# Performance work log

Hardware: AMD Instinct MI355X
Metric: run time of the kernel (lower is better)

Reference implementation:

```python
import jax, jax.numpy as jnp
import numpy as np

N_NODES = 50000
N_EDGES = 800000
IN_FEAT = 128
OUT_FEAT = 128


def setup_inputs() -> dict:
    key = jax.random.key(0)
    ks = jax.random.split(key, 12)
    s = lambda fan_in: 1.0 / np.sqrt(fan_in)
    inp = {
        "node_feats": jax.random.normal(ks[0], (N_NODES, IN_FEAT), dtype=jnp.float32),
        "edge_feats": jax.random.normal(ks[1], (N_EDGES, IN_FEAT), dtype=jnp.float32),
        "src": jax.random.randint(ks[2], (N_EDGES,), 0, N_NODES),
        "dst": jax.random.randint(ks[3], (N_EDGES,), 0, N_NODES),
        # mlp1: Linear(2*in -> in), ReLU, Linear(in -> in)
        "W1a": jax.random.uniform(ks[4], (2 * IN_FEAT, IN_FEAT), jnp.float32, -s(2 * IN_FEAT), s(2 * IN_FEAT)),
        "b1a": jnp.zeros((IN_FEAT,), jnp.float32),
        "W1b": jax.random.uniform(ks[5], (IN_FEAT, IN_FEAT), jnp.float32, -s(IN_FEAT), s(IN_FEAT)),
        "b1b": jnp.zeros((IN_FEAT,), jnp.float32),
        # mlp2: Linear(in -> out), ReLU, Linear(out -> out)
        "W2a": jax.random.uniform(ks[6], (IN_FEAT, OUT_FEAT), jnp.float32, -s(IN_FEAT), s(IN_FEAT)),
        "b2a": jnp.zeros((OUT_FEAT,), jnp.float32),
        "W2b": jax.random.uniform(ks[7], (OUT_FEAT, OUT_FEAT), jnp.float32, -s(OUT_FEAT), s(OUT_FEAT)),
        "b2b": jnp.zeros((OUT_FEAT,), jnp.float32),
    }
    return inp


def reference(node_feats, edge_feats, src, dst, W1a, b1a, W1b, b1b, W2a, b2a, W2b, b2b):
    # message: mlp1(cat([h_src, e]))  -> [E, in_feat]
    cat = jnp.concatenate([node_feats[src], edge_feats], axis=1)  # [E, 2*in]
    m = jax.nn.relu(cat @ W1a + b1a) @ W1b + b1b                  # [E, in]
    # reduce: scatter-sum over dst + residual
    agg = jax.ops.segment_sum(m, dst, num_segments=node_feats.shape[0])
    h = agg + node_feats                                          # [N, in]
    # mlp2
    out = jax.nn.relu(h @ W2a + b2a) @ W2b + b2b                  # [N, out]
    return out
```

## Files before the change

kernel.cpp:

```cpp
#include <hip/hip_runtime.h>
#include <hip/hip_bf16.h>

typedef __attribute__((ext_vector_type(8))) short short8;
typedef __attribute__((ext_vector_type(4))) float floatx4;
typedef unsigned short ushort_t;

#define MFMA(a, b, c) __builtin_amdgcn_mfma_f32_16x16x32_bf16((a), (b), (c), 0, 0, 0)

constexpr int N_NODES = 50000;
constexpr int N_EDGES = 800000;
constexpr int EDGE_BLOCKS = N_EDGES / 32;
constexpr int NODE_TILES = (N_NODES + 63) / 64;
constexpr int YS_STRIDE = 136;
constexpr int MS_STRIDE = 132;

__device__ __forceinline__ unsigned short f2b(float x) {
  union { float f; unsigned u; } c; c.f = x;
  unsigned r = c.u + 0x7FFFu + ((c.u >> 16) & 1u);
  return (unsigned short)(r >> 16);
}

__device__ __forceinline__ unsigned pk2(float x, float y) {
  __hip_bfloat162 h = __float22bfloat162_rn(float2{x, y});
  unsigned u; __builtin_memcpy(&u, &h, 4);
  return u;
}

__device__ __forceinline__ short8 mk_frag(const float4 a, const float4 b) {
  union { short8 s; unsigned u[4]; } r;
  r.u[0] = pk2(a.x, a.y); r.u[1] = pk2(a.z, a.w);
  r.u[2] = pk2(b.x, b.y); r.u[3] = pk2(b.z, b.w);
  return r.s;
}

__global__ void prep(const float* __restrict__ W1a, const float* __restrict__ W1b,
                     const float* __restrict__ W2a, const float* __restrict__ W2b,
                     ushort_t* __restrict__ wbuf, float4* __restrict__ agg4,
                     unsigned* __restrict__ cnt) {
  const int t = blockIdx.x * blockDim.x + threadIdx.x;
  const int stride = gridDim.x * blockDim.x;
  const float4 z = {0.f, 0.f, 0.f, 0.f};
  for (int i = t; i < N_NODES * 32; i += stride) agg4[i] = z;
  for (int i = t; i < N_NODES; i += stride) cnt[i] = 0u;

  ushort_t* W1s1 = wbuf;
  ushort_t* W1s2 = wbuf + 32768;
  ushort_t* W2aT = wbuf + 49152;
  ushort_t* W2bT = wbuf + 65536;

  for (int i = t; i < 32768; i += stride) {
    const int j = i & 7, lane = (i >> 3) & 63, fb = i >> 9;
    const int ks = fb >> 3, nt = fb & 7;
    const int k = ks * 32 + (lane >> 4) * 8 + j, n = nt * 16 + (lane & 15);
    W1s1[i] = f2b(W1a[k * 128 + n]);
  }
  for (int i = t; i < 16384; i += stride) {
    const int j = i & 7, lane = (i >> 3) & 63, fb = i >> 9;
    const int ks = fb >> 3, nt = fb & 7;
    const int k = ks * 32 + (lane >> 4) * 8 + j, n = nt * 16 + (lane & 15);
    W1s2[i] = f2b(W1b[k * 128 + n]);
  }
  for (int i = t; i < 16384; i += stride) {
    const int n = i >> 7, k = i & 127;
    W2aT[i] = f2b(W2a[k * 128 + n]);
    W2bT[i] = f2b(W2b[k * 128 + n]);
  }
}

__global__ void hist_dst(const int* __restrict__ dst, unsigned* __restrict__ cnt) {
  int i = blockIdx.x * blockDim.x + threadIdx.x;
  const int stride = gridDim.x * blockDim.x;
  for (; i < N_EDGES; i += stride) atomicAdd(&cnt[dst[i]], 1u);
}

__global__ __launch_bounds__(1024) void scan_cnt(unsigned* __restrict__ cnt) {
  __shared__ unsigned wsum[16];
  __shared__ unsigned carry_s;
  const int tid = threadIdx.x;
  const int lane = tid & 63, wv = tid >> 6;
  if (tid == 0) carry_s = 0u;
  __syncthreads();
  for (int base = 0; base < N_NODES; base += 1024) {
    const int i = base + tid;
    const unsigned v = (i < N_NODES) ? cnt[i] : 0u;
    unsigned s = v;
#pragma unroll
    for (int off = 1; off < 64; off <<= 1) {
      unsigned t = __shfl_up(s, off);
      if (lane >= off) s += t;
    }
    if (lane == 63) wsum[wv] = s;
    __syncthreads();
    if (wv == 0 && lane < 16) {
      unsigned w = wsum[lane];
      unsigned sw = w;
#pragma unroll
      for (int off = 1; off < 16; off <<= 1) {
        unsigned t = __shfl_up(sw, off);
        if (lane >= off) sw += t;
      }
      wsum[lane] = sw - w;
    }
    __syncthreads();
    const unsigned excl = s - v + wsum[wv] + carry_s;
    if (i < N_NODES) cnt[i] = excl;
    __syncthreads();
    if (tid == 1023) carry_s = excl + v;
    __syncthreads();
  }
}

__global__ void scatter_idx(const int* __restrict__ dst, unsigned* __restrict__ cnt,
                            unsigned* __restrict__ perm) {
  int i = blockIdx.x * blockDim.x + threadIdx.x;
  const int stride = gridDim.x * blockDim.x;
  for (; i < N_EDGES; i += stride) {
    const unsigned pos = atomicAdd(&cnt[dst[i]], 1u);
    perm[pos] = (unsigned)i;
  }
}

__global__ __launch_bounds__(64, 4) void edge_mlp(
    const float* __restrict__ nf, const float* __restrict__ ef,
    const int* __restrict__ src, const int* __restrict__ dst,
    const unsigned* __restrict__ perm,
    const float* __restrict__ b1a, const float* __restrict__ b1b,
    const ushort_t* __restrict__ W1s1, const ushort_t* __restrict__ W1s2,
    float* __restrict__ agg) {
  __shared__ __align__(16) char smem[32 * MS_STRIDE * 4];
  ushort_t* Ys = (ushort_t*)smem;
  float* Ms = (float*)smem;

  const int lane = threadIdx.x;
  const int l16 = lane & 15;
  const int quad = lane >> 4;
  const int tb = blockIdx.x * 32;

  int dlane = 0;
  if (lane < 32) dlane = dst[perm[tb + lane]];

  const int e0 = (int)perm[tb + l16];
  const int e1 = (int)perm[tb + 16 + l16];
  const int s0 = src[e0];
  const int s1 = src[e1];

  floatx4 acc[2][8];
#pragma unroll
  for (int nt = 0; nt < 8; ++nt) {
    const float bz = b1a[nt * 16 + l16];
    acc[0][nt] = (floatx4){bz, bz, bz, bz};
    acc[1][nt] = acc[0][nt];
  }
#pragma unroll
  for (int ks = 0; ks < 8; ++ks) {
    short8 a0, a1;
    if (ks < 4) {
      const float4* p0 = (const float4*)nf + (long)s0 * 32 + ks * 8 + quad * 2;
      const float4* p1 = (const float4*)nf + (long)s1 * 32 + ks * 8 + quad * 2;
      a0 = mk_frag(p0[0], p0[1]);
      a1 = mk_frag(p1[0], p1[1]);
    } else {
      const float4* p0 = (const float4*)ef + (long)e0 * 32 + (ks - 4) * 8 + quad * 2;
      const float4* p1 = (const float4*)ef + (long)e1 * 32 + (ks - 4) * 8 + quad * 2;
      a0 = mk_frag(p0[0], p0[1]);
      a1 = mk_frag(p1[0], p1[1]);
    }
    short8 bfr[8];
#pragma unroll
    for (int nt = 0; nt < 8; ++nt)
      bfr[nt] = *(const short8*)(W1s1 + ((ks * 8 + nt) * 64 + lane) * 8);
#pragma unroll
    for (int nt = 0; nt < 8; ++nt) {
      acc[0][nt] = MFMA(a0, bfr[nt], acc[0][nt]);
      acc[1][nt] = MFMA(a1, bfr[nt], acc[1][nt]);
    }
  }

#pragma unroll
  for (int mt = 0; mt < 2; ++mt)
#pragma unroll
    for (int nt = 0; nt < 8; ++nt)
#pragma unroll
      for (int r = 0; r < 4; ++r)
        Ys[(mt * 16 + quad * 4 + r) * YS_STRIDE + nt * 16 + l16] =
            f2b(fmaxf(acc[mt][nt][r], 0.f));

  floatx4 acc2[2][8];
#pragma unroll
  for (int nt = 0; nt < 8; ++nt) {
    const float bz = b1b[nt * 16 + l16];
    acc2[0][nt] = (floatx4){bz, bz, bz, bz};
    acc2[1][nt] = acc2[0][nt];
  }
#pragma unroll
  for (int ks = 0; ks < 4; ++ks) {
    const short8 a0 = *(const short8*)(&Ys[l16 * YS_STRIDE + ks * 32 + quad * 8]);
    const short8 a1 = *(const short8*)(&Ys[(16 + l16) * YS_STRIDE + ks * 32 + quad * 8]);
    short8 bfr[8];
#pragma unroll
    for (int nt = 0; nt < 8; ++nt)
      bfr[nt] = *(const short8*)(W1s2 + ((ks * 8 + nt) * 64 + lane) * 8);
#pragma unroll
    for (int nt = 0; nt < 8; ++nt) {
      acc2[0][nt] = MFMA(a0, bfr[nt], acc2[0][nt]);
      acc2[1][nt] = MFMA(a1, bfr[nt], acc2[1][nt]);
    }
  }

#pragma unroll
  for (int mt = 0; mt < 2; ++mt)
#pragma unroll
    for (int nt = 0; nt < 8; ++nt)
#pragma unroll
      for (int r = 0; r < 4; ++r)
        Ms[(mt * 16 + quad * 4 + r) * MS_STRIDE + nt * 16 + l16] = acc2[mt][nt][r];

  float a0 = 0.f, a1 = 0.f;
  int cur = __shfl(dlane, 0);
  for (int r = 0; r < 32; ++r) {
    const int d = __shfl(dlane, r);
    if (d != cur) {
      unsafeAtomicAdd(&agg[(long)cur * 128 + lane], a0);
      unsafeAtomicAdd(&agg[(long)cur * 128 + 64 + lane], a1);
      a0 = 0.f; a1 = 0.f; cur = d;
    }
    a0 += Ms[r * MS_STRIDE + lane];
    a1 += Ms[r * MS_STRIDE + 64 + lane];
  }
  unsafeAtomicAdd(&agg[(long)cur * 128 + lane], a0);
  unsafeAtomicAdd(&agg[(long)cur * 128 + 64 + lane], a1);
}

__global__ __launch_bounds__(256) void node_mlp(
    const float* __restrict__ nf, const float* __restrict__ agg,
    const float* __restrict__ b2a, const float* __restrict__ b2b,
    const ushort_t* __restrict__ W2aT, const ushort_t* __restrict__ W2bT,
    float* __restrict__ out) {
  __shared__ __align__(16) ushort_t Xs[64 * YS_STRIDE];
  __shared__ __align__(16) ushort_t Ys2[64 * YS_STRIDE];

  const int tid = threadIdx.x;
  const int wave = tid >> 6;
  const int lane = tid & 63;
  const int l16 = lane & 15;
  const int quad = lane >> 4;
  const int nbase = wave * 32;
  const int rbase = blockIdx.x * 64;

  short8 bfrA[2][4], bfrB[2][4];
  float biasA[2], biasB[2];
#pragma unroll
  for (int t = 0; t < 2; ++t) {
    const int n = nbase + t * 16 + l16;
#pragma unroll
    for (int ks = 0; ks < 4; ++ks) {
      bfrA[t][ks] = *(const short8*)(W2aT + n * 128 + ks * 32 + quad * 8);
      bfrB[t][ks] = *(const short8*)(W2bT + n * 128 + ks * 32 + quad * 8);
    }
    biasA[t] = b2a[n];
    biasB[t] = b2b[n];
  }

#pragma unroll
  for (int i = 0; i < 8; ++i) {
    const int fidx = tid + 256 * i;
    const int r = fidx >> 5;
    const int c4 = fidx & 31;
    const long gr = min(rbase + r, N_NODES - 1);
    const float4 a = ((const float4*)agg)[gr * 32 + c4];
    const float4 n = ((const float4*)nf)[gr * 32 + c4];
    unsigned* p = (unsigned*)&Xs[r * YS_STRIDE + c4 * 4];
    p[0] = pk2(a.x + n.x, a.y + n.y);
    p[1] = pk2(a.z + n.z, a.w + n.w);
  }
  __syncthreads();

  floatx4 acc[4][2];
#pragma unroll
  for (int mt = 0; mt < 4; ++mt)
#pragma unroll
    for (int t = 0; t < 2; ++t)
      acc[mt][t] = (floatx4){biasA[t], biasA[t], biasA[t], biasA[t]};
#pragma unroll
  for (int ks = 0; ks < 4; ++ks)
#pragma unroll
    for (int mt = 0; mt < 4; ++mt) {
      const short8 a = *(const short8*)(&Xs[(mt * 16 + l16) * YS_STRIDE + ks * 32 + quad * 8]);
      acc[mt][0] = MFMA(a, bfrA[0][ks], acc[mt][0]);
      acc[mt][1] = MFMA(a, bfrA[1][ks], acc[mt][1]);
    }
#pragma unroll
  for (int mt = 0; mt < 4; ++mt)
#pragma unroll
    for (int t = 0; t < 2; ++t)
#pragma unroll
      for (int r = 0; r < 4; ++r) {
        const int row = mt * 16 + quad * 4 + r;
        const int col = nbase + t * 16 + l16;
        Ys2[row * YS_STRIDE + col] = f2b(fmaxf(acc[mt][t][r], 0.f));
      }
  __syncthreads();

  floatx4 acc2[4][2];
#pragma unroll
  for (int mt = 0; mt < 4; ++mt)
#pragma unroll
    for (int t = 0; t < 2; ++t)
      acc2[mt][t] = (floatx4){biasB[t], biasB[t], biasB[t], biasB[t]};
#pragma unroll
  for (int ks = 0; ks < 4; ++ks)
#pragma unroll
    for (int mt = 0; mt < 4; ++mt) {
      const short8 a = *(const short8*)(&Ys2[(mt * 16 + l16) * YS_STRIDE + ks * 32 + quad * 8]);
      acc2[mt][0] = MFMA(a, bfrB[0][ks], acc2[mt][0]);
      acc2[mt][1] = MFMA(a, bfrB[1][ks], acc2[mt][1]);
    }
#pragma unroll
  for (int mt = 0; mt < 4; ++mt)
#pragma unroll
    for (int t = 0; t < 2; ++t)
#pragma unroll
      for (int r = 0; r < 4; ++r) {
        const int row = mt * 16 + quad * 4 + r;
        const int grow = rbase + row;
        if (grow < N_NODES) {
          const int col = nbase + t * 16 + l16;
          out[(long)grow * 128 + col] = acc2[mt][t][r];
        }
      }
}

extern "C" void kernel_launch(void* const* d_in, const int* in_sizes, int n_in,
                              void* d_out, int out_size, void* d_ws, size_t ws_size,
                              hipStream_t stream) {
  const float* nf = (const float*)d_in[0];
  const float* ef = (const float*)d_in[1];
  const int* src = (const int*)d_in[2];
  const int* dst = (const int*)d_in[3];
  const float* W1a = (const float*)d_in[4];
  const float* b1a = (const float*)d_in[5];
  const float* W1b = (const float*)d_in[6];
  const float* b1b = (const float*)d_in[7];
  const float* W2a = (const float*)d_in[8];
  const float* b2a = (const float*)d_in[9];
  const float* W2b = (const float*)d_in[10];
  const float* b2b = (const float*)d_in[11];
  float* out = (float*)d_out;

  char* ws = (char*)d_ws;
  float* agg = (float*)ws;
  ushort_t* wbuf = (ushort_t*)(ws + 25600000);
  const ushort_t* W1s1 = wbuf;
  const ushort_t* W1s2 = wbuf + 32768;
  const ushort_t* W2aT = wbuf + 49152;
  const ushort_t* W2bT = wbuf + 65536;

  unsigned* cnt = (unsigned*)out;
  unsigned* perm = (unsigned*)out + 65536;

  prep<<<1024, 256, 0, stream>>>(W1a, W1b, W2a, W2b, wbuf, (float4*)agg, cnt);
  hist_dst<<<1024, 256, 0, stream>>>(dst, cnt);
  scan_cnt<<<1, 1024, 0, stream>>>(cnt);
  scatter_idx<<<1024, 256, 0, stream>>>(dst, cnt, perm);
  edge_mlp<<<EDGE_BLOCKS, 64, 0, stream>>>(nf, ef, src, dst, perm, b1a, b1b, W1s1, W1s2, agg);
  node_mlp<<<NODE_TILES, 256, 0, stream>>>(nf, agg, b2a, b2b, W2aT, W2bT, out);
}
```

Measured before the change: 933.8 us.

## Parallelize dst prefix scan and reduce edge segments in registers via ballot

Replaces the single-block serial exclusive scan over node counts with a three-kernel multi-block scan (per-block scan, block-sum scan, add-back). In the edge MLP, the LDS staging of the second-layer output and the per-row serial segmented sum are replaced by a ballot that finds dst-run boundaries, followed by register masking and cross-quad shuffles to form per-segment sums. Atomic adds are then issued per segment. Perm indices are loaded once per lane and broadcast with shuffles. The register reduction re-walks all accumulators once per segment, which costs more when a 32-edge block spans many distinct destinations. With random destinations most segments hold only one or two edges.

```diff
diff --git a/kernel.cpp b/kernel.cpp
--- a/kernel.cpp
+++ b/kernel.cpp
@@ -11,8 +11,8 @@
 constexpr int N_EDGES = 800000;
 constexpr int EDGE_BLOCKS = N_EDGES / 32;
 constexpr int NODE_TILES = (N_NODES + 63) / 64;
+constexpr int SCAN_BLOCKS = (N_NODES + 1023) / 1024;
 constexpr int YS_STRIDE = 136;
-constexpr int MS_STRIDE = 132;
 
 __device__ __forceinline__ unsigned short f2b(float x) {
   union { float f; unsigned u; } c; c.f = x;
@@ -73,41 +73,50 @@
   for (; i < N_EDGES; i += stride) atomicAdd(&cnt[dst[i]], 1u);
 }
 
-__global__ __launch_bounds__(1024) void scan_cnt(unsigned* __restrict__ cnt) {
+__global__ __launch_bounds__(1024) void scan1(unsigned* __restrict__ cnt,
+                                              unsigned* __restrict__ bsum) {
   __shared__ unsigned wsum[16];
-  __shared__ unsigned carry_s;
-  const int tid = threadIdx.x;
-  const int lane = tid & 63, wv = tid >> 6;
-  if (tid == 0) carry_s = 0u;
+  const int tid = threadIdx.x, lane = tid & 63, wv = tid >> 6;
+  const int i = blockIdx.x * 1024 + tid;
+  const unsigned v = (i < N_NODES) ? cnt[i] : 0u;
+  unsigned s = v;
+#pragma unroll
+  for (int off = 1; off < 64; off <<= 1) {
+    unsigned t = __shfl_up(s, off);
+    if (lane >= off) s += t;
+  }
+  if (lane == 63) wsum[wv] = s;
   __syncthreads();
-  for (int base = 0; base < N_NODES; base += 1024) {
-    const int i = base + tid;
-    const unsigned v = (i < N_NODES) ? cnt[i] : 0u;
-    unsigned s = v;
-#pragma unroll
-    for (int off = 1; off < 64; off <<= 1) {
-      unsigned t = __shfl_up(s, off);
-      if (lane >= off) s += t;
-    }
-    if (lane == 63) wsum[wv] = s;
-    __syncthreads();
-    if (wv == 0 && lane < 16) {
-      unsigned w = wsum[lane];
-      unsigned sw = w;
-#pragma unroll
-      for (int off = 1; off < 16; off <<= 1) {
-        unsigned t = __shfl_up(sw, off);
-        if (lane >= off) sw += t;
-      }
-      wsum[lane] = sw - w;
-    }
-    __syncthreads();
-    const unsigned excl = s - v + wsum[wv] + carry_s;
-    if (i < N_NODES) cnt[i] = excl;
-    __syncthreads();
-    if (tid == 1023) carry_s = excl + v;
-    __syncthreads();
-  }
+  if (wv == 0 && lane < 16) {
+    unsigned w = wsum[lane], sw = w;
+#pragma unroll
+    for (int off = 1; off < 16; off <<= 1) {
+      unsigned t = __shfl_up(sw, off);
+      if (lane >= off) sw += t;
+    }
+    wsum[lane] = sw - w;
+    if (lane == 15) bsum[blockIdx.x] = sw;
+  }
+  __syncthreads();
+  if (i < N_NODES) cnt[i] = s - v + wsum[wv];
+}
+
+__global__ void scan2(unsigned* __restrict__ bsum) {
+  const int lane = threadIdx.x;
+  const unsigned v = (lane < SCAN_BLOCKS) ? bsum[lane] : 0u;
+  unsigned s = v;
+#pragma unroll
+  for (int off = 1; off < 64; off <<= 1) {
+    unsigned t = __shfl_up(s, off);
+    if (lane >= off) s += t;
+  }
+  if (lane < SCAN_BLOCKS) bsum[lane] = s - v;
+}
+
+__global__ __launch_bounds__(1024) void scan3(unsigned* __restrict__ cnt,
+                                              const unsigned* __restrict__ bsum) {
+  const int i = blockIdx.x * 1024 + threadIdx.x;
+  if (i < N_NODES) cnt[i] += bsum[blockIdx.x];
 }
 
 __global__ void scatter_idx(const int* __restrict__ dst, unsigned* __restrict__ cnt,
@@ -127,20 +136,20 @@
     const float* __restrict__ b1a, const float* __restrict__ b1b,
     const ushort_t* __restrict__ W1s1, const ushort_t* __restrict__ W1s2,
     float* __restrict__ agg) {
-  __shared__ __align__(16) char smem[32 * MS_STRIDE * 4];
-  ushort_t* Ys = (ushort_t*)smem;
-  float* Ms = (float*)smem;
+  __shared__ __align__(16) ushort_t Ys[32 * YS_STRIDE];
 
   const int lane = threadIdx.x;
   const int l16 = lane & 15;
   const int quad = lane >> 4;
   const int tb = blockIdx.x * 32;
 
+  int plane = 0;
+  if (lane < 32) plane = (int)perm[tb + lane];
   int dlane = 0;
-  if (lane < 32) dlane = dst[perm[tb + lane]];
-
-  const int e0 = (int)perm[tb + l16];
-  const int e1 = (int)perm[tb + 16 + l16];
+  if (lane < 32) dlane = dst[plane];
+
+  const int e0 = __shfl(plane, l16);
+  const int e1 = __shfl(plane, 16 + l16);
   const int s0 = src[e0];
   const int s1 = src[e1];
 
@@ -207,28 +216,42 @@
     }
   }
 
-#pragma unroll
-  for (int mt = 0; mt < 2; ++mt)
-#pragma unroll
-    for (int nt = 0; nt < 8; ++nt)
-#pragma unroll
-      for (int r = 0; r < 4; ++r)
-        Ms[(mt * 16 + quad * 4 + r) * MS_STRIDE + nt * 16 + l16] = acc2[mt][nt][r];
-
-  float a0 = 0.f, a1 = 0.f;
-  int cur = __shfl(dlane, 0);
-  for (int r = 0; r < 32; ++r) {
-    const int d = __shfl(dlane, r);
-    if (d != cur) {
-      unsafeAtomicAdd(&agg[(long)cur * 128 + lane], a0);
-      unsafeAtomicAdd(&agg[(long)cur * 128 + 64 + lane], a1);
-      a0 = 0.f; a1 = 0.f; cur = d;
-    }
-    a0 += Ms[r * MS_STRIDE + lane];
-    a1 += Ms[r * MS_STRIDE + 64 + lane];
-  }
-  unsafeAtomicAdd(&agg[(long)cur * 128 + lane], a0);
-  unsafeAtomicAdd(&agg[(long)cur * 128 + 64 + lane], a1);
+  const int dprev = __shfl_up(dlane, 1);
+  const bool flag = (lane == 0) || (dlane != dprev);
+  const unsigned long long m = __ballot(flag) & 0xFFFFFFFFull;
+
+  int lo = 0;
+  while (true) {
+    const unsigned long long rest = m >> (lo + 1);
+    const int hi = rest ? (lo + 1 + __builtin_ctzll(rest)) : 32;
+    const int d = __shfl(dlane, lo);
+
+    float s[8];
+#pragma unroll
+    for (int nt = 0; nt < 8; ++nt) s[nt] = 0.f;
+#pragma unroll
+    for (int mt = 0; mt < 2; ++mt)
+#pragma unroll
+      for (int r = 0; r < 4; ++r) {
+        const int row = mt * 16 + quad * 4 + r;
+        const bool in = (row >= lo) && (row < hi);
+#pragma unroll
+        for (int nt = 0; nt < 8; ++nt)
+          s[nt] += in ? acc2[mt][nt][r] : 0.f;
+      }
+#pragma unroll
+    for (int nt = 0; nt < 8; ++nt) {
+      s[nt] += __shfl_xor(s[nt], 16);
+      s[nt] += __shfl_xor(s[nt], 32);
+    }
+    const float v0 = quad == 0 ? s[0] : quad == 1 ? s[2] : quad == 2 ? s[4] : s[6];
+    const float v1 = quad == 0 ? s[1] : quad == 1 ? s[3] : quad == 2 ? s[5] : s[7];
+    unsafeAtomicAdd(&agg[(long)d * 128 + quad * 32 + l16], v0);
+    unsafeAtomicAdd(&agg[(long)d * 128 + quad * 32 + 16 + l16], v1);
+
+    if (hi >= 32) break;
+    lo = hi;
+  }
 }
 
 __global__ __launch_bounds__(256) void node_mlp(
@@ -357,10 +380,13 @@
 
   unsigned* cnt = (unsigned*)out;
   unsigned* perm = (unsigned*)out + 65536;
+  unsigned* bsum = (unsigned*)out + 65536 + 800000;
 
   prep<<<1024, 256, 0, stream>>>(W1a, W1b, W2a, W2b, wbuf, (float4*)agg, cnt);
   hist_dst<<<1024, 256, 0, stream>>>(dst, cnt);
-  scan_cnt<<<1, 1024, 0, stream>>>(cnt);
+  scan1<<<SCAN_BLOCKS, 1024, 0, stream>>>(cnt, bsum);
+  scan2<<<1, 64, 0, stream>>>(bsum);
+  scan3<<<SCAN_BLOCKS, 1024, 0, stream>>>(cnt, bsum);
   scatter_idx<<<1024, 256, 0, stream>>>(dst, cnt, perm);
   edge_mlp<<<EDGE_BLOCKS, 64, 0, stream>>>(nf, ef, src, dst, perm, b1a, b1b, W1s1, W1s2, agg);
   node_mlp<<<NODE_TILES, 256, 0, stream>>>(nf, agg, b2a, b2b, W2aT, W2bT, out);
```

After: 858.2 us. 1.09x faster.
